# Kernel optimization log

Measured on AMD Instinct MI355X. Metric: run time of the kernel, lower is better.

The kernel has to match this reference:

```python
import jax, jax.numpy as jnp
import numpy as np

D, M, N = 1024, 16, 16384
H = D // M  # head dim = 64
C = 10.0    # tanh logit clipping


def setup_inputs() -> dict:
    key = jax.random.key(0)
    kb, kq, km, k1, k2, k3, k4 = jax.random.split(key, 7)
    def xavier(k, shape):
        # torch xavier_uniform: fan_in = prod(shape[1:]), fan_out = shape[0]*prod(shape[2:])
        fan_in = int(np.prod(shape[1:]))
        fan_out = shape[0] * int(np.prod(shape[2:]))
        bound = float(np.sqrt(6.0 / (fan_in + fan_out)))
        return jax.random.uniform(k, shape, jnp.float32, -bound, bound)
    return {
        "b": jax.random.normal(kb, (N, D), jnp.float32),
        "q_s_bar": jax.random.normal(kq, (D,), jnp.float32),
        "mask": jax.random.randint(km, (N,), 0, 2).astype(bool),
        "W_k_bar": xavier(k1, (M, H, D)),
        "W_v_bar": xavier(k2, (M, H, D)),
        "W_k": xavier(k3, (D, D)),
        "W_q": xavier(k4, (D, D)),
    }


def reference(b, q_s_bar, mask, W_k_bar, W_v_bar, W_k, W_q):
    # k_bar, v_bar: (N, M, H)  == matmul(W, b.t()).permute(2,0,1)
    k_bar = jnp.einsum('mhd,nd->nmh', W_k_bar, b)
    v_bar = jnp.einsum('mhd,nd->nmh', W_v_bar, b)
    k = b @ W_k.T                      # (N, D) == matmul(W_k, b.t()).t()
    q = q_s_bar.reshape(M, H)          # (M, H)
    # c_bar: (N, M, M) == matmul(k_bar, q.T) / sqrt(h)
    c_bar = jnp.einsum('nmh,gh->nmg', k_bar, q) / np.float32(np.sqrt(H))
    scores = jnp.where(mask[:, None, None], c_bar, -jnp.inf)
    attn = jax.nn.softmax(scores, axis=0)          # softmax over N
    # (N,M,M) @ (N,M,H) batched -> (N,M,H); view(N,-1).sum(0) -> (D,)
    q_s = jnp.einsum('nmg,ngh->nmh', attn, v_bar).reshape(N, D).sum(0)
    c = (k @ (W_q @ q_s)) / np.float32(np.sqrt(D))  # (N,)
    c = C * jnp.tanh(c)
    return jnp.where(mask, c, -jnp.inf)
```

## Files before the change

### kernel.cpp

```cpp
#include <hip/hip_runtime.h>
#include <math.h>
#include <float.h>

#define NN 16384
#define DD 1024
#define MM 16
#define HH 64
#define MG 256

typedef __attribute__((ext_vector_type(8))) short bh8;
typedef __attribute__((ext_vector_type(4))) float f32x4;

__device__ inline float bf2f(unsigned short u) {
    union { unsigned int i; float f; } v;
    v.i = ((unsigned int)u) << 16;
    return v.f;
}

__device__ inline unsigned short f2bf(float f) {
    union { float f; unsigned int i; } v;
    v.f = f;
    unsigned int r = v.i + 0x7FFFu + ((v.i >> 16) & 1u);
    return (unsigned short)(r >> 16);
}

__device__ inline float ld1(const void* p, long i, int isf) {
    return isf ? ((const float*)p)[i] : bf2f(((const unsigned short*)p)[i]);
}

__device__ inline float4 ld4(const void* p, long i, int isf) {
    if (isf) return *(const float4*)((const float*)p + i);
    ushort4 u = *(const ushort4*)((const unsigned short*)p + i);
    return make_float4(bf2f(u.x), bf2f(u.y), bf2f(u.z), bf2f(u.w));
}

__device__ inline bool get_mask(const unsigned char* mp, int n, int flag) {
    return flag ? (mp[n] != 0) : (mp[4 * n] != 0);
}

__device__ inline void gl_lds16(const void* g, void* l) {
    __builtin_amdgcn_global_load_lds(
        (const __attribute__((address_space(1))) unsigned int*)g,
        (__attribute__((address_space(3))) unsigned int*)l, 16, 0, 0);
}

__global__ void detect(const unsigned char* __restrict__ mp,
                       const unsigned char* __restrict__ bb, int* flags,
                       float* __restrict__ u) {
    int i = blockIdx.x * 256 + threadIdx.x;
    if (i < DD) u[i] = 0.f;
    int v1 = ((i & 3) != 0 && mp[i] != 0) ? 1 : 0;
    unsigned char c = bb[4 * i + 1];
    bool expish = (c == 0x00) || (c == 0x80) || (c >= 0x30 && c <= 0x47) ||
                  (c >= 0xB0 && c <= 0xC7);
    int v2 = expish ? 0 : 1;
    unsigned long long b1 = __ballot(v1);
    unsigned long long b2 = __ballot(v2);
    if ((threadIdx.x & 63) == 0) {
        if (b1) atomicOr(&flags[0], 1);
        if (b2) atomicOr(&flags[1], 1);
    }
}

__global__ void fold_k(const void* __restrict__ Wkb, const void* __restrict__ qsb,
                       unsigned short* __restrict__ Abf, const int* __restrict__ flags) {
    __shared__ float q[DD];
    int isf = flags[1];
    int m = blockIdx.x;
    int d = blockIdx.y * 128 + threadIdx.x;
    for (int i = threadIdx.x; i < DD; i += 128) q[i] = ld1(qsb, i, isf);
    __syncthreads();
    float acc[MM];
#pragma unroll
    for (int g = 0; g < MM; g++) acc[g] = 0.f;
    for (int h = 0; h < HH; h++) {
        float w = ld1(Wkb, (long)(m * HH + h) * DD + d, isf);
#pragma unroll
        for (int g = 0; g < MM; g++) acc[g] += w * q[g * HH + h];
    }
#pragma unroll
    for (int g = 0; g < MM; g++)
        Abf[(long)(m * MM + g) * DD + d] = f2bf(acc[g] * 0.125f);
}

__global__ void cvt_b(const void* __restrict__ bB, unsigned short* __restrict__ bbf,
                      unsigned short* __restrict__ bT, const int* __restrict__ flags) {
    __shared__ unsigned int tl[128 * 32];
    int isf = flags[1];
    int bn = blockIdx.x, bd = blockIdx.y;
    int t = threadIdx.x;
    int i = t >> 1, h = t & 1;
    long gbase = (long)(bn * 128 + i) * DD + bd * 64 + h * 32;
    unsigned int pk[16];
    if (isf) {
        const float* src = (const float*)bB + gbase;
#pragma unroll
        for (int k = 0; k < 8; k++) {
            float4 f = *(const float4*)(src + k * 4);
            pk[k * 2] = (unsigned int)f2bf(f.x) | ((unsigned int)f2bf(f.y) << 16);
            pk[k * 2 + 1] = (unsigned int)f2bf(f.z) | ((unsigned int)f2bf(f.w) << 16);
        }
    } else {
        const unsigned int* src = (const unsigned int*)((const unsigned short*)bB + gbase);
#pragma unroll
        for (int k = 0; k < 16; k++) pk[k] = src[k];
    }
#pragma unroll
    for (int k = 0; k < 4; k++)
        *(uint4*)&bbf[gbase + k * 8] =
            make_uint4(pk[4 * k], pk[4 * k + 1], pk[4 * k + 2], pk[4 * k + 3]);
#pragma unroll
    for (int m = 0; m < 16; m++)
        tl[i * 32 + ((16 * h + m) ^ (i & 31))] = pk[m];
    __syncthreads();
    const unsigned short* us = (const unsigned short*)tl;
#pragma unroll
    for (int iter = 0; iter < 2; iter++) {
        int pl = iter * 32 + (t >> 3);
        int g = t & 7;
#pragma unroll
        for (int half = 0; half < 2; half++) {
            int nb = half * 64 + g * 8;
            bh8 o;
#pragma unroll
            for (int jj = 0; jj < 8; jj++) {
                int n = nb + jj;
                int dw = n * 32 + ((pl >> 1) ^ (n & 31));
                o[jj] = (short)us[dw * 2 + (pl & 1)];
            }
            *(bh8*)&bT[(long)(bd * 64 + pl) * NN + bn * 128 + nb] = o;
        }
    }
}

__global__ __launch_bounds__(256) void gemm_b_mfma(
    const unsigned short* __restrict__ Abf, const unsigned short* __restrict__ bbf,
    const unsigned char* __restrict__ mp, const int* __restrict__ flags,
    unsigned short* __restrict__ Cb) {
    __shared__ __align__(16) unsigned short As[128 * 64];
    __shared__ __align__(16) unsigned short Bs[64 * 64];
    int m0 = blockIdx.x * 128, n0 = blockIdx.y * 64;
    int t = threadIdx.x;
    int lane = t & 63, w = t >> 6;
    int wm = w >> 1, wn = w & 1;
    int r = lane & 15, q = lane >> 4;
    f32x4 acc[4][2] = {};
    for (int k0 = 0; k0 < DD; k0 += 64) {
#pragma unroll
        for (int i = 0; i < 4; i++) {
            int L = (i * 4 + w) * 64 + lane;
            int row = L >> 3, c = (L & 7) ^ (row & 7);
            gl_lds16(&Abf[(long)(m0 + row) * DD + k0 + c * 8], &As[(i * 4 + w) * 512]);
        }
#pragma unroll
        for (int i = 0; i < 2; i++) {
            int L = (i * 4 + w) * 64 + lane;
            int row = L >> 3, c = (L & 7) ^ (row & 7);
            gl_lds16(&bbf[(long)(n0 + row) * DD + k0 + c * 8], &Bs[(i * 4 + w) * 512]);
        }
        __syncthreads();
#pragma unroll
        for (int h = 0; h < 2; h++) {
            bh8 af[4], bfr[2];
#pragma unroll
            for (int fi = 0; fi < 4; fi++) {
                int row = wm * 64 + fi * 16 + r;
                int ck = (h * 4 + q) ^ (row & 7);
                af[fi] = *(const bh8*)&As[row * 64 + ck * 8];
            }
#pragma unroll
            for (int fj = 0; fj < 2; fj++) {
                int row = wn * 32 + fj * 16 + r;
                int ck = (h * 4 + q) ^ (row & 7);
                bfr[fj] = *(const bh8*)&Bs[row * 64 + ck * 8];
            }
#pragma unroll
            for (int fi = 0; fi < 4; fi++)
#pragma unroll
                for (int fj = 0; fj < 2; fj++)
                    acc[fi][fj] = __builtin_amdgcn_mfma_f32_16x16x32_bf16(
                        af[fi], bfr[fj], acc[fi][fj], 0, 0, 0);
        }
        __syncthreads();
    }
    int mflag = flags[0];
#pragma unroll
    for (int fj = 0; fj < 2; fj++) {
        int gn = n0 + wn * 32 + fj * 16 + r;
        float nb = get_mask(mp, gn, mflag) ? 0.f : -INFINITY;
#pragma unroll
        for (int fi = 0; fi < 4; fi++)
#pragma unroll
            for (int reg = 0; reg < 4; reg++) {
                int gm = m0 + wm * 64 + fi * 16 + q * 4 + reg;
                Cb[(long)gm * NN + gn] = f2bf(acc[fi][fj][reg] + nb);
            }
    }
}

__global__ void softmax_part(const unsigned short* __restrict__ Cb,
                             float* __restrict__ sws) {
    __shared__ float red[256];
    int mg = blockIdx.x, z = blockIdx.y, t = threadIdx.x;
    bh8 v8 = *(const bh8*)&Cb[(long)mg * NN + z * 2048 + t * 8];
    float x[8];
#pragma unroll
    for (int j = 0; j < 8; j++) x[j] = bf2f((unsigned short)v8[j]);
    float mx = x[0];
#pragma unroll
    for (int j = 1; j < 8; j++) mx = fmaxf(mx, x[j]);
    red[t] = mx;
    __syncthreads();
    for (int s = 128; s; s >>= 1) {
        if (t < s) red[t] = fmaxf(red[t], red[t + s]);
        __syncthreads();
    }
    mx = red[0];
    __syncthreads();
    float sm = 0.f;
#pragma unroll
    for (int j = 0; j < 8; j++) sm += expf(x[j] - mx);
    red[t] = sm;
    __syncthreads();
    for (int s = 128; s; s >>= 1) {
        if (t < s) red[t] += red[t + s];
        __syncthreads();
    }
    if (t == 0) {
        sws[(mg * 8 + z) * 2] = mx;
        sws[(mg * 8 + z) * 2 + 1] = red[0];
    }
}

__global__ void softmax_norm(const unsigned short* __restrict__ Cb,
                             const float* __restrict__ sws,
                             unsigned short* __restrict__ P) {
    int mg = blockIdx.x, z = blockIdx.y, t = threadIdx.x;
    float mx = -INFINITY;
#pragma unroll
    for (int z2 = 0; z2 < 8; z2++) mx = fmaxf(mx, sws[(mg * 8 + z2) * 2]);
    float S = 0.f;
#pragma unroll
    for (int z2 = 0; z2 < 8; z2++) {
        float pm = sws[(mg * 8 + z2) * 2], ps = sws[(mg * 8 + z2) * 2 + 1];
        if (pm > -INFINITY) S += ps * expf(pm - mx);
    }
    float inv = 1.0f / S;
    long i = (long)mg * NN + z * 2048 + t * 8;
    bh8 v8 = *(const bh8*)&Cb[i];
    bh8 o;
#pragma unroll
    for (int j = 0; j < 8; j++)
        o[j] = (short)f2bf(expf(bf2f((unsigned short)v8[j]) - mx) * inv);
    *(bh8*)&P[i] = o;
}

__global__ __launch_bounds__(256) void gemm_d_mfma(
    const unsigned short* __restrict__ P, const unsigned short* __restrict__ bT,
    unsigned short* __restrict__ Tpart) {
    __shared__ __align__(16) unsigned short As[128 * 64];
    __shared__ __align__(16) unsigned short Bs[64 * 64];
    int m0 = blockIdx.x * 128, d0 = blockIdx.y * 64;
    long kbase = (long)blockIdx.z * 1024;
    unsigned short* Cg = Tpart + (long)blockIdx.z * (MG * DD);
    int t = threadIdx.x;
    int lane = t & 63, w = t >> 6;
    int wm = w >> 1, wn = w & 1;
    int r = lane & 15, q = lane >> 4;
    f32x4 acc[4][2] = {};
    for (int k0 = 0; k0 < 1024; k0 += 64) {
#pragma unroll
        for (int i = 0; i < 4; i++) {
            int L = (i * 4 + w) * 64 + lane;
            int row = L >> 3, c = (L & 7) ^ (row & 7);
            gl_lds16(&P[(long)(m0 + row) * NN + kbase + k0 + c * 8], &As[(i * 4 + w) * 512]);
        }
#pragma unroll
        for (int i = 0; i < 2; i++) {
            int L = (i * 4 + w) * 64 + lane;
            int row = L >> 3, c = (L & 7) ^ (row & 7);
            gl_lds16(&bT[(long)(d0 + row) * NN + kbase + k0 + c * 8], &Bs[(i * 4 + w) * 512]);
        }
        __syncthreads();
#pragma unroll
        for (int h = 0; h < 2; h++) {
            bh8 af[4], bfr[2];
#pragma unroll
            for (int fi = 0; fi < 4; fi++) {
                int row = wm * 64 + fi * 16 + r;
                int ck = (h * 4 + q) ^ (row & 7);
                af[fi] = *(const bh8*)&As[row * 64 + ck * 8];
            }
#pragma unroll
            for (int fj = 0; fj < 2; fj++) {
                int row = wn * 32 + fj * 16 + r;
                int ck = (h * 4 + q) ^ (row & 7);
                bfr[fj] = *(const bh8*)&Bs[row * 64 + ck * 8];
            }
#pragma unroll
            for (int fi = 0; fi < 4; fi++)
#pragma unroll
                for (int fj = 0; fj < 2; fj++)
                    acc[fi][fj] = __builtin_amdgcn_mfma_f32_16x16x32_bf16(
                        af[fi], bfr[fj], acc[fi][fj], 0, 0, 0);
        }
        __syncthreads();
    }
#pragma unroll
    for (int fi = 0; fi < 4; fi++)
#pragma unroll
        for (int fj = 0; fj < 2; fj++)
#pragma unroll
            for (int reg = 0; reg < 4; reg++) {
                int gm = m0 + wm * 64 + fi * 16 + q * 4 + reg;
                int gd = d0 + wn * 32 + fj * 16 + r;
                Cg[(long)gm * DD + gd] = f2bf(acc[fi][fj][reg]);
            }
}

__global__ void reduce_T(const unsigned short* __restrict__ Tpart, float* __restrict__ T) {
    long i = (long)(blockIdx.x * 256 + threadIdx.x) * 8;
    float s[8] = {};
#pragma unroll
    for (int c = 0; c < 16; c++) {
        bh8 v = *(const bh8*)&Tpart[(long)c * (MG * DD) + i];
#pragma unroll
        for (int j = 0; j < 8; j++) s[j] += bf2f((unsigned short)v[j]);
    }
    *(float4*)&T[i] = make_float4(s[0], s[1], s[2], s[3]);
    *(float4*)&T[i + 4] = make_float4(s[4], s[5], s[6], s[7]);
}

__global__ void fold_v(const void* __restrict__ Wvb, const float* __restrict__ T,
                       float* __restrict__ qs, const int* __restrict__ flags) {
    int isf = flags[1];
    int w = threadIdx.x >> 6, lane = threadIdx.x & 63;
    int o = blockIdx.x * 4 + w;
    int m = o >> 6, h = o & 63;
    float s = 0.f;
    for (int g = 0; g < MM; g++) {
        const float* Trow = T + (long)(m * MM + g) * DD;
        long wbase = (long)(g * HH + h) * DD;
#pragma unroll
        for (int k = 0; k < 4; k++) {
            int d = lane * 4 + k * 256;
            float4 tv = *(const float4*)&Trow[d];
            float4 wv = ld4(Wvb, wbase + d, isf);
            s += wv.x * tv.x + wv.y * tv.y + wv.z * tv.z + wv.w * tv.w;
        }
    }
    for (int off = 32; off; off >>= 1) s += __shfl_down(s, off, 64);
    if (lane == 0) qs[o] = s;
}

__global__ void matvec_rows(const void* __restrict__ W, const float* __restrict__ x,
                            float* __restrict__ y, const int* __restrict__ flags) {
    int isf = flags[1];
    int lane = threadIdx.x & 63;
    int r = blockIdx.x * 4 + (threadIdx.x >> 6);
    long base = (long)r * DD;
    float s = 0.f;
#pragma unroll
    for (int k = 0; k < 4; k++) {
        int j = lane * 4 + k * 256;
        float4 wv = ld4(W, base + j, isf);
        float4 xv = *(const float4*)&x[j];
        s += wv.x * xv.x + wv.y * xv.y + wv.z * xv.z + wv.w * xv.w;
    }
    for (int off = 32; off; off >>= 1) s += __shfl_down(s, off, 64);
    if (lane == 0) y[r] = s;
}

__global__ void matvec_col(const void* __restrict__ Wk, const float* __restrict__ w1,
                           float* __restrict__ u, const int* __restrict__ flags) {
    __shared__ float xs[16];
    int isf = flags[1];
    int d = blockIdx.x * 256 + threadIdx.x;
    int i0 = blockIdx.y * 16;
    if (threadIdx.x < 16) xs[threadIdx.x] = w1[i0 + threadIdx.x];
    __syncthreads();
    float s = 0.f;
#pragma unroll
    for (int ii = 0; ii < 16; ii++) s += ld1(Wk, (long)(i0 + ii) * DD + d, isf) * xs[ii];
    atomicAdd(&u[d], s);
}

__global__ void final_k(const unsigned short* __restrict__ bbf, const float* __restrict__ u,
                        const unsigned char* __restrict__ mp, const int* __restrict__ flags,
                        void* __restrict__ out) {
    int mflag = flags[0];
    int isf = flags[1];
    int n = blockIdx.x * 4 + (threadIdx.x >> 6);
    int lane = threadIdx.x & 63;
    const unsigned short* row = bbf + (long)n * DD;
    float s = 0.f;
#pragma unroll
    for (int k = 0; k < 4; k++) {
        int j = lane * 4 + k * 256;
        ushort4 v = *(const ushort4*)&row[j];
        float4 uu = *(const float4*)&u[j];
        s += bf2f(v.x) * uu.x + bf2f(v.y) * uu.y + bf2f(v.z) * uu.z + bf2f(v.w) * uu.w;
    }
    for (int off = 32; off; off >>= 1) s += __shfl_down(s, off, 64);
    if (lane == 0) {
        float c = 10.f * tanhf(s * (1.0f / 32.0f));
        bool mk = get_mask(mp, n, mflag);
        if (isf) {
            union { unsigned int i; float f; } vv;
            vv.i = mk ? (((unsigned int)f2bf(c)) << 16) : 0xFF7F0000u;
            ((float*)out)[n] = vv.f;
        } else {
            ((unsigned short*)out)[n] = mk ? f2bf(c) : (unsigned short)0xFF7F;
        }
    }
}

extern "C" void kernel_launch(void* const* d_in, const int* in_sizes, int n_in,
                              void* d_out, int out_size, void* d_ws, size_t ws_size,
                              hipStream_t stream) {
    const void* b = d_in[0];
    const void* qsb = d_in[1];
    const unsigned char* mp = (const unsigned char*)d_in[2];
    const void* Wkb = d_in[3];
    const void* Wvb = d_in[4];
    const void* Wk = d_in[5];
    const void* Wq = d_in[6];

    char* ws = (char*)d_ws;
    unsigned short* bbf = (unsigned short*)(ws);
    unsigned short* bT = (unsigned short*)(ws + (32u << 20));
    unsigned short* Cb = (unsigned short*)(ws + (64u << 20));
    unsigned short* Tpart = (unsigned short*)(ws + (72u << 20));
    unsigned short* P = (unsigned short*)(ws + (80u << 20));
    unsigned short* Abf = (unsigned short*)(ws + (88u << 20));
    float* T = (float*)(ws + (89u << 20));
    float* small = (float*)(ws + (90u << 20));
    float* qs = small;
    float* w1 = qs + 1024;
    float* u = w1 + 1024;
    float* sws = u + 1024;
    int* flags = (int*)(sws + 4096);

    hipMemsetAsync(flags, 0, 2 * sizeof(int), stream);

    detect<<<64, 256, 0, stream>>>(mp, (const unsigned char*)b, flags, u);
    fold_k<<<dim3(16, 8), 128, 0, stream>>>(Wkb, qsb, Abf, flags);
    cvt_b<<<dim3(128, 16), 256, 0, stream>>>(b, bbf, bT, flags);
    gemm_b_mfma<<<dim3(2, 256), 256, 0, stream>>>(Abf, bbf, mp, flags, Cb);
    softmax_part<<<dim3(256, 8), 256, 0, stream>>>(Cb, sws);
    softmax_norm<<<dim3(256, 8), 256, 0, stream>>>(Cb, sws, P);
    gemm_d_mfma<<<dim3(2, 16, 16), 256, 0, stream>>>(P, bT, Tpart);
    reduce_T<<<128, 256, 0, stream>>>(Tpart, T);
    fold_v<<<256, 256, 0, stream>>>(Wvb, T, qs, flags);
    matvec_rows<<<256, 256, 0, stream>>>(Wq, qs, w1, flags);
    matvec_col<<<dim3(4, 64), 256, 0, stream>>>(Wk, w1, u, flags);
    final_k<<<4096, 256, 0, stream>>>(bbf, u, mp, flags, d_out);
}
```

Before: 234.3 us.

## Split b conversion into coalesced bf16 cast and separate transpose kernel

The fused convert-and-transpose kernel is split in two. The first is a fully coalesced fp32-to-bf16 cast in which each thread handles 16 contiguous elements. The second reads the bf16 copy back and transposes 64x64 tiles through padded shared memory. fold_k also gets smaller blocks (64 threads) and twice as many of them, for more parallelism. The intent is better memory coalescing and occupancy, at the cost of an extra launch and an extra 32MB read of the bf16 buffer.

```diff
diff --git a/kernel.cpp b/kernel.cpp
--- a/kernel.cpp
+++ b/kernel.cpp
@@ -67,8 +67,8 @@
     __shared__ float q[DD];
     int isf = flags[1];
     int m = blockIdx.x;
-    int d = blockIdx.y * 128 + threadIdx.x;
-    for (int i = threadIdx.x; i < DD; i += 128) q[i] = ld1(qsb, i, isf);
+    int d = blockIdx.y * 64 + threadIdx.x;
+    for (int i = threadIdx.x; i < DD; i += 64) q[i] = ld1(qsb, i, isf);
     __syncthreads();
     float acc[MM];
 #pragma unroll
@@ -83,53 +83,50 @@
         Abf[(long)(m * MM + g) * DD + d] = f2bf(acc[g] * 0.125f);
 }
 
-__global__ void cvt_b(const void* __restrict__ bB, unsigned short* __restrict__ bbf,
-                      unsigned short* __restrict__ bT, const int* __restrict__ flags) {
-    __shared__ unsigned int tl[128 * 32];
-    int isf = flags[1];
-    int bn = blockIdx.x, bd = blockIdx.y;
-    int t = threadIdx.x;
-    int i = t >> 1, h = t & 1;
-    long gbase = (long)(bn * 128 + i) * DD + bd * 64 + h * 32;
-    unsigned int pk[16];
+__global__ void cvt_bbf(const void* __restrict__ bB, unsigned short* __restrict__ bbf,
+                        const int* __restrict__ flags) {
+    int isf = flags[1];
+    long base = ((long)blockIdx.x * 256 + threadIdx.x) * 16;
+    unsigned int pk[8];
     if (isf) {
-        const float* src = (const float*)bB + gbase;
-#pragma unroll
-        for (int k = 0; k < 8; k++) {
+        const float* src = (const float*)bB + base;
+#pragma unroll
+        for (int k = 0; k < 4; k++) {
             float4 f = *(const float4*)(src + k * 4);
             pk[k * 2] = (unsigned int)f2bf(f.x) | ((unsigned int)f2bf(f.y) << 16);
             pk[k * 2 + 1] = (unsigned int)f2bf(f.z) | ((unsigned int)f2bf(f.w) << 16);
         }
     } else {
-        const unsigned int* src = (const unsigned int*)((const unsigned short*)bB + gbase);
-#pragma unroll
-        for (int k = 0; k < 16; k++) pk[k] = src[k];
-    }
-#pragma unroll
-    for (int k = 0; k < 4; k++)
-        *(uint4*)&bbf[gbase + k * 8] =
-            make_uint4(pk[4 * k], pk[4 * k + 1], pk[4 * k + 2], pk[4 * k + 3]);
-#pragma unroll
-    for (int m = 0; m < 16; m++)
-        tl[i * 32 + ((16 * h + m) ^ (i & 31))] = pk[m];
-    __syncthreads();
-    const unsigned short* us = (const unsigned short*)tl;
-#pragma unroll
-    for (int iter = 0; iter < 2; iter++) {
-        int pl = iter * 32 + (t >> 3);
-        int g = t & 7;
-#pragma unroll
-        for (int half = 0; half < 2; half++) {
-            int nb = half * 64 + g * 8;
-            bh8 o;
-#pragma unroll
-            for (int jj = 0; jj < 8; jj++) {
-                int n = nb + jj;
-                int dw = n * 32 + ((pl >> 1) ^ (n & 31));
-                o[jj] = (short)us[dw * 2 + (pl & 1)];
-            }
-            *(bh8*)&bT[(long)(bd * 64 + pl) * NN + bn * 128 + nb] = o;
-        }
+        const uint4* src = (const uint4*)((const unsigned short*)bB + base);
+        uint4 a = src[0], b4 = src[1];
+        pk[0] = a.x; pk[1] = a.y; pk[2] = a.z; pk[3] = a.w;
+        pk[4] = b4.x; pk[5] = b4.y; pk[6] = b4.z; pk[7] = b4.w;
+    }
+    *(uint4*)&bbf[base] = make_uint4(pk[0], pk[1], pk[2], pk[3]);
+    *(uint4*)&bbf[base + 8] = make_uint4(pk[4], pk[5], pk[6], pk[7]);
+}
+
+__global__ void cvt_bT(const unsigned short* __restrict__ bbf,
+                       unsigned short* __restrict__ bT) {
+    __shared__ unsigned short tl[64 * 68];
+    int bn = blockIdx.x, bd = blockIdx.y;
+    int t = threadIdx.x;
+    int r = t >> 3, g = t & 7;
+#pragma unroll
+    for (int pass = 0; pass < 2; pass++) {
+        int row = pass * 32 + r;
+        bh8 v = *(const bh8*)&bbf[(long)(bn * 64 + row) * DD + bd * 64 + g * 8];
+        *(bh8*)&tl[row * 68 + g * 8] = v;
+    }
+    __syncthreads();
+#pragma unroll
+    for (int pass = 0; pass < 2; pass++) {
+        int d = pass * 32 + r;
+        int nb = g * 8;
+        bh8 o;
+#pragma unroll
+        for (int j = 0; j < 8; j++) o[j] = (short)tl[(nb + j) * 68 + d];
+        *(bh8*)&bT[(long)(bd * 64 + d) * NN + bn * 64 + nb] = o;
     }
 }
 
@@ -444,8 +441,9 @@
     hipMemsetAsync(flags, 0, 2 * sizeof(int), stream);
 
     detect<<<64, 256, 0, stream>>>(mp, (const unsigned char*)b, flags, u);
-    fold_k<<<dim3(16, 8), 128, 0, stream>>>(Wkb, qsb, Abf, flags);
-    cvt_b<<<dim3(128, 16), 256, 0, stream>>>(b, bbf, bT, flags);
+    fold_k<<<dim3(16, 16), 64, 0, stream>>>(Wkb, qsb, Abf, flags);
+    cvt_bbf<<<4096, 256, 0, stream>>>(b, bbf, flags);
+    cvt_bT<<<dim3(256, 16), 256, 0, stream>>>(bbf, bT);
     gemm_b_mfma<<<dim3(2, 256), 256, 0, stream>>>(Abf, bbf, mp, flags, Cb);
     softmax_part<<<dim3(256, 8), 256, 0, stream>>>(Cb, sws);
     softmax_norm<<<dim3(256, 8), 256, 0, stream>>>(Cb, sws, P);
```

Result: faster. 229.2 us (-2.2%).
